# Kernel optimization log

Hardware: AMD Instinct MI355X
Metric: run time of the kernel (lower is better)

## Reference

```python
import jax, jax.numpy as jnp
import numpy as np
import hashlib

VOCAB = 50257
EMBED_DIM = 2048
STEPS = 8
B, L = 4, 8192


def _c_tables(vocab):
    # Precompute the deterministic SHA-256-derived Julia constants per token id,
    # exactly matching FractalEmbedding._token_to_c.
    cr = np.empty(vocab, dtype=np.float32)
    ci = np.empty(vocab, dtype=np.float32)
    for t in range(vocab):
        h = hashlib.sha256(str(t).encode()).hexdigest()
        cr[t] = (int(h[:16], 16) / 2**64 - 0.5) * 2.0
        ci[t] = (int(h[16:32], 16) / 2**64 - 0.5) * 2.0
    return jnp.asarray(cr), jnp.asarray(ci)


def setup_inputs() -> dict:
    key = jax.random.key(0)
    k_tok, k_w = jax.random.split(key)
    token_ids = jax.random.randint(k_tok, (B, L), 0, VOCAB, dtype=jnp.int64)
    c_real, c_imag = _c_tables(VOCAB)
    # nn.Linear(2*steps, embed_dim, bias=False): kaiming-uniform, bound = 1/sqrt(16)
    bound = 1.0 / np.sqrt(2 * STEPS)
    proj_w = jax.random.uniform(k_w, (EMBED_DIM, 2 * STEPS), jnp.float32, -bound, bound)
    scale = jnp.ones((), jnp.float32)
    return {"token_ids": token_ids, "c_real": c_real, "c_imag": c_imag,
            "proj_w": proj_w, "scale": scale}


def reference(token_ids, c_real, c_imag, proj_w, scale):
    # Gather per-token Julia constants: [B, L]
    cr = c_real[token_ids]
    ci = c_imag[token_ids]
    zr = jnp.zeros_like(cr)
    zi = jnp.zeros_like(ci)
    feats = []  # interleaved (real, imag) per step -> 2*STEPS features
    for _ in range(STEPS):
        zr, zi = zr * zr - zi * zi + cr, 2.0 * zr * zi + ci
        feats.append(zr)
        feats.append(zi)
    feats = jnp.stack(feats, axis=-1)  # [B, L, 2*STEPS]
    out = jnp.einsum('blf,df->bld', feats, proj_w) * scale  # [B, L, EMBED_DIM]
    return out
```

## Files before the change

### kernel.cpp

```cpp
#include <hip/hip_runtime.h>


constexpr int TOKENS = 4 * 8192;
constexpr int EMBED  = 2048;
constexpr int NF     = 16;
constexpr int STEPS  = 8;
constexpr int TB     = 64;

typedef float f32x2 __attribute__((ext_vector_type(2)));
typedef float f32x4 __attribute__((ext_vector_type(4)));

__global__ __launch_bounds__(256, 2)
void fused_kernel(const int* __restrict__ tok,
                  const float* __restrict__ crt,
                  const float* __restrict__ cit,
                  const float* __restrict__ W,
                  const float* __restrict__ scale_p,
                  float* __restrict__ out)
{
    const int tid  = threadIdx.x;
    const int dlo  = tid * 4;
    const int dhi  = 1024 + tid * 4;
    const float s  = scale_p[0];

    f32x2 wp[2][2][NF];
    #pragma unroll
    for (int c = 0; c < 2; ++c) {
        const int d = (c == 0) ? dlo : dhi;
        const f32x4* W4 = reinterpret_cast<const f32x4*>(W + (size_t)d * NF);
        #pragma unroll
        for (int p = 0; p < 2; ++p) {
            #pragma unroll
            for (int k = 0; k < 4; ++k) {
                f32x4 a = W4[p * 8 + k];
                f32x4 b = W4[p * 8 + 4 + k];
                wp[c][p][4 * k + 0] = (f32x2){ a.x * s, b.x * s };
                wp[c][p][4 * k + 1] = (f32x2){ a.y * s, b.y * s };
                wp[c][p][4 * k + 2] = (f32x2){ a.z * s, b.z * s };
                wp[c][p][4 * k + 3] = (f32x2){ a.w * s, b.w * s };
            }
        }
    }

    __shared__ float feats[TB][NF];
    const int tok0 = blockIdx.x * TB;
    if (tid < TB) {
        const int t = tok[tok0 + tid];
        const float cr = crt[t];
        const float ci = cit[t];
        float zr = 0.0f, zi = 0.0f;
        #pragma unroll
        for (int st = 0; st < STEPS; ++st) {
            const float nzr = zr * zr - zi * zi + cr;
            const float nzi = 2.0f * zr * zi + ci;
            zr = nzr; zi = nzi;
            feats[tid][2 * st]     = zr;
            feats[tid][2 * st + 1] = zi;
        }
    }
    __syncthreads();

    float* __restrict__ olo = out + (size_t)tok0 * EMBED + dlo;
    float* __restrict__ ohi = out + (size_t)tok0 * EMBED + dhi;

    for (int i = 0; i < TB; i += 2) {
        float fa[NF], fb[NF];
        {
            const f32x4* fpa = reinterpret_cast<const f32x4*>(feats[i]);
            const f32x4* fpb = reinterpret_cast<const f32x4*>(feats[i + 1]);
            #pragma unroll
            for (int k = 0; k < 4; ++k) {
                f32x4 va = fpa[k], vb = fpb[k];
                fa[4 * k + 0] = va.x; fa[4 * k + 1] = va.y;
                fa[4 * k + 2] = va.z; fa[4 * k + 3] = va.w;
                fb[4 * k + 0] = vb.x; fb[4 * k + 1] = vb.y;
                fb[4 * k + 2] = vb.z; fb[4 * k + 3] = vb.w;
            }
        }
        f32x2 aL0 = {0.f,0.f}, aL1 = {0.f,0.f}, aH0 = {0.f,0.f}, aH1 = {0.f,0.f};
        f32x2 bL0 = {0.f,0.f}, bL1 = {0.f,0.f}, bH0 = {0.f,0.f}, bH1 = {0.f,0.f};
        #pragma unroll
        for (int k = 0; k < NF; ++k) {
            const f32x2 fA = { fa[k], fa[k] };
            const f32x2 fB = { fb[k], fb[k] };
            aL0 += fA * wp[0][0][k];
            aL1 += fA * wp[0][1][k];
            aH0 += fA * wp[1][0][k];
            aH1 += fA * wp[1][1][k];
            bL0 += fB * wp[0][0][k];
            bL1 += fB * wp[0][1][k];
            bH0 += fB * wp[1][0][k];
            bH1 += fB * wp[1][1][k];
        }
        const size_t r0 = (size_t)i * EMBED;
        const size_t r1 = (size_t)(i + 1) * EMBED;
        *reinterpret_cast<f32x4*>(olo + r0) = (f32x4){ aL0.x, aL0.y, aL1.x, aL1.y };
        *reinterpret_cast<f32x4*>(ohi + r0) = (f32x4){ aH0.x, aH0.y, aH1.x, aH1.y };
        *reinterpret_cast<f32x4*>(olo + r1) = (f32x4){ bL0.x, bL0.y, bL1.x, bL1.y };
        *reinterpret_cast<f32x4*>(ohi + r1) = (f32x4){ bH0.x, bH0.y, bH1.x, bH1.y };
    }
}

extern "C" void kernel_launch(void* const* d_in, const int* in_sizes, int n_in,
                              void* d_out, int out_size, void* d_ws, size_t ws_size,
                              hipStream_t stream) {
    const int*   tok   = (const int*)d_in[0];
    const float* crt   = (const float*)d_in[1];
    const float* cit   = (const float*)d_in[2];
    const float* W     = (const float*)d_in[3];
    const float* scale = (const float*)d_in[4];
    float*       out   = (float*)d_out;

    fused_kernel<<<TOKENS / TB, 256, 0, stream>>>(tok, crt, cit, W, scale, out);
}
```

Before: 53.01 us.

## Split feature computation into a separate kernel writing to workspace

Splits the fused kernel into two launches. A small kernel computes the per-token Julia iteration features into a workspace buffer, and a projection kernel reads them straight from global memory instead of shared memory. This removes the per-block gather, the idle-thread feature phase and the __syncthreads barrier from the store-bound projection. In exchange it adds a second kernel launch and a 2 MB round trip through global memory. The original fused kernel is kept as a fallback when the workspace is too small.

```diff
diff --git a/kernel.cpp b/kernel.cpp
--- a/kernel.cpp
+++ b/kernel.cpp
@@ -10,18 +10,44 @@
 typedef float f32x2 __attribute__((ext_vector_type(2)));
 typedef float f32x4 __attribute__((ext_vector_type(4)));
 
-__global__ __launch_bounds__(256, 2)
-void fused_kernel(const int* __restrict__ tok,
+__global__ __launch_bounds__(64)
+void feats_kernel(const int* __restrict__ tok,
                   const float* __restrict__ crt,
                   const float* __restrict__ cit,
-                  const float* __restrict__ W,
-                  const float* __restrict__ scale_p,
-                  float* __restrict__ out)
+                  float* __restrict__ feats)
 {
-    const int tid  = threadIdx.x;
-    const int dlo  = tid * 4;
-    const int dhi  = 1024 + tid * 4;
-    const float s  = scale_p[0];
+    const int t = blockIdx.x * 64 + threadIdx.x;
+    const int id = tok[t];
+    const float cr = crt[id];
+    const float ci = cit[id];
+    float f[NF];
+    float zr = 0.0f, zi = 0.0f;
+    #pragma unroll
+    for (int st = 0; st < STEPS; ++st) {
+        const float nzr = zr * zr - zi * zi + cr;
+        const float nzi = 2.0f * zr * zi + ci;
+        zr = nzr; zi = nzi;
+        f[2 * st]     = zr;
+        f[2 * st + 1] = zi;
+    }
+    f32x4* fo = reinterpret_cast<f32x4*>(feats + (size_t)t * NF);
+    #pragma unroll
+    for (int j = 0; j < 4; ++j) {
+        f32x4 v = { f[4 * j], f[4 * j + 1], f[4 * j + 2], f[4 * j + 3] };
+        fo[j] = v;
+    }
+}
+
+__global__ __launch_bounds__(256, 2)
+void proj_kernel(const float* __restrict__ feats,
+                 const float* __restrict__ W,
+                 const float* __restrict__ scale_p,
+                 float* __restrict__ out)
+{
+    const int tid = threadIdx.x;
+    const int dlo = tid * 4;
+    const int dhi = 1024 + tid * 4;
+    const float s = scale_p[0];
 
     f32x2 wp[2][2][NF];
     #pragma unroll
@@ -42,32 +68,16 @@
         }
     }
 
-    __shared__ float feats[TB][NF];
     const int tok0 = blockIdx.x * TB;
-    if (tid < TB) {
-        const int t = tok[tok0 + tid];
-        const float cr = crt[t];
-        const float ci = cit[t];
-        float zr = 0.0f, zi = 0.0f;
-        #pragma unroll
-        for (int st = 0; st < STEPS; ++st) {
-            const float nzr = zr * zr - zi * zi + cr;
-            const float nzi = 2.0f * zr * zi + ci;
-            zr = nzr; zi = nzi;
-            feats[tid][2 * st]     = zr;
-            feats[tid][2 * st + 1] = zi;
-        }
-    }
-    __syncthreads();
-
+    const float* fbase = feats + (size_t)tok0 * NF;
     float* __restrict__ olo = out + (size_t)tok0 * EMBED + dlo;
     float* __restrict__ ohi = out + (size_t)tok0 * EMBED + dhi;
 
     for (int i = 0; i < TB; i += 2) {
         float fa[NF], fb[NF];
         {
-            const f32x4* fpa = reinterpret_cast<const f32x4*>(feats[i]);
-            const f32x4* fpb = reinterpret_cast<const f32x4*>(feats[i + 1]);
+            const f32x4* fpa = reinterpret_cast<const f32x4*>(fbase + i * NF);
+            const f32x4* fpb = reinterpret_cast<const f32x4*>(fbase + (i + 1) * NF);
             #pragma unroll
             for (int k = 0; k < 4; ++k) {
                 f32x4 va = fpa[k], vb = fpb[k];
@@ -101,6 +111,91 @@
     }
 }
 
+__global__ __launch_bounds__(256, 2)
+void fused_kernel(const int* __restrict__ tok,
+                  const float* __restrict__ crt,
+                  const float* __restrict__ cit,
+                  const float* __restrict__ W,
+                  const float* __restrict__ scale_p,
+                  float* __restrict__ out)
+{
+    const int tid = threadIdx.x;
+    const int dlo = tid * 4;
+    const int dhi = 1024 + tid * 4;
+    const float s = scale_p[0];
+    f32x2 wp[2][2][NF];
+    #pragma unroll
+    for (int c = 0; c < 2; ++c) {
+        const int d = (c == 0) ? dlo : dhi;
+        const f32x4* W4 = reinterpret_cast<const f32x4*>(W + (size_t)d * NF);
+        #pragma unroll
+        for (int p = 0; p < 2; ++p) {
+            #pragma unroll
+            for (int k = 0; k < 4; ++k) {
+                f32x4 a = W4[p * 8 + k];
+                f32x4 b = W4[p * 8 + 4 + k];
+                wp[c][p][4 * k + 0] = (f32x2){ a.x * s, b.x * s };
+                wp[c][p][4 * k + 1] = (f32x2){ a.y * s, b.y * s };
+                wp[c][p][4 * k + 2] = (f32x2){ a.z * s, b.z * s };
+                wp[c][p][4 * k + 3] = (f32x2){ a.w * s, b.w * s };
+            }
+        }
+    }
+    __shared__ float feats[TB][NF];
+    const int tok0 = blockIdx.x * TB;
+    if (tid < TB) {
+        const int t = tok[tok0 + tid];
+        const float cr = crt[t], ci = cit[t];
+        float zr = 0.0f, zi = 0.0f;
+        #pragma unroll
+        for (int st = 0; st < STEPS; ++st) {
+            const float nzr = zr * zr - zi * zi + cr;
+            const float nzi = 2.0f * zr * zi + ci;
+            zr = nzr; zi = nzi;
+            feats[tid][2 * st] = zr; feats[tid][2 * st + 1] = zi;
+        }
+    }
+    __syncthreads();
+    float* __restrict__ olo = out + (size_t)tok0 * EMBED + dlo;
+    float* __restrict__ ohi = out + (size_t)tok0 * EMBED + dhi;
+    for (int i = 0; i < TB; i += 2) {
+        float fa[NF], fb[NF];
+        {
+            const f32x4* fpa = reinterpret_cast<const f32x4*>(feats[i]);
+            const f32x4* fpb = reinterpret_cast<const f32x4*>(feats[i + 1]);
+            #pragma unroll
+            for (int k = 0; k < 4; ++k) {
+                f32x4 va = fpa[k], vb = fpb[k];
+                fa[4 * k + 0] = va.x; fa[4 * k + 1] = va.y;
+                fa[4 * k + 2] = va.z; fa[4 * k + 3] = va.w;
+                fb[4 * k + 0] = vb.x; fb[4 * k + 1] = vb.y;
+                fb[4 * k + 2] = vb.z; fb[4 * k + 3] = vb.w;
+            }
+        }
+        f32x2 aL0 = {0.f,0.f}, aL1 = {0.f,0.f}, aH0 = {0.f,0.f}, aH1 = {0.f,0.f};
+        f32x2 bL0 = {0.f,0.f}, bL1 = {0.f,0.f}, bH0 = {0.f,0.f}, bH1 = {0.f,0.f};
+        #pragma unroll
+        for (int k = 0; k < NF; ++k) {
+            const f32x2 fA = { fa[k], fa[k] };
+            const f32x2 fB = { fb[k], fb[k] };
+            aL0 += fA * wp[0][0][k];
+            aL1 += fA * wp[0][1][k];
+            aH0 += fA * wp[1][0][k];
+            aH1 += fA * wp[1][1][k];
+            bL0 += fB * wp[0][0][k];
+            bL1 += fB * wp[0][1][k];
+            bH0 += fB * wp[1][0][k];
+            bH1 += fB * wp[1][1][k];
+        }
+        const size_t r0 = (size_t)i * EMBED;
+        const size_t r1 = (size_t)(i + 1) * EMBED;
+        *reinterpret_cast<f32x4*>(olo + r0) = (f32x4){ aL0.x, aL0.y, aL1.x, aL1.y };
+        *reinterpret_cast<f32x4*>(ohi + r0) = (f32x4){ aH0.x, aH0.y, aH1.x, aH1.y };
+        *reinterpret_cast<f32x4*>(olo + r1) = (f32x4){ bL0.x, bL0.y, bL1.x, bL1.y };
+        *reinterpret_cast<f32x4*>(ohi + r1) = (f32x4){ bH0.x, bH0.y, bH1.x, bH1.y };
+    }
+}
+
 extern "C" void kernel_launch(void* const* d_in, const int* in_sizes, int n_in,
                               void* d_out, int out_size, void* d_ws, size_t ws_size,
                               hipStream_t stream) {
@@ -111,5 +206,12 @@
     const float* scale = (const float*)d_in[4];
     float*       out   = (float*)d_out;
 
-    fused_kernel<<<TOKENS / TB, 256, 0, stream>>>(tok, crt, cit, W, scale, out);
-}
+    const size_t feats_bytes = (size_t)TOKENS * NF * sizeof(float);
+    if (ws_size >= feats_bytes) {
+        float* feats = (float*)d_ws;
+        feats_kernel<<<TOKENS / 64, 64, 0, stream>>>(tok, crt, cit, feats);
+        proj_kernel<<<TOKENS / TB, 256, 0, stream>>>(feats, W, scale, out);
+    } else {
+        fused_kernel<<<TOKENS / TB, 256, 0, stream>>>(tok, crt, cit, W, scale, out);
+    }
+}
```

Result: slower. 57.60 us (+8.7%).
